# Optimization experiments

Hardware: AMD Instinct MI355X
Metric: run time of the kernel (lower is better)

## Reference

```python
import jax, jax.numpy as jnp
import numpy as np

BS, NS, D, H = 4, 1024, 2048, 16
DH = D // H
SCALE = DH ** -0.5
MASK_BIAS = -1e9


def setup_inputs() -> dict:
    key = jax.random.key(0)
    k1, k2, k3, k4, k5 = jax.random.split(key, 5)
    x = jax.random.normal(k1, (BS, NS, D), dtype=jnp.float32)
    attention_ids = jax.random.randint(k2, (BS, NS), 0, 2, dtype=jnp.int32)
    # torch.nn.Linear weights: [out_features, in_features]
    w_in = jax.random.normal(k3, (3 * D, D), dtype=jnp.float32) * (D ** -0.5)
    w_out = jax.random.normal(k4, (D, D), dtype=jnp.float32) * (D ** -0.5)
    b_out = jax.random.normal(k5, (D,), dtype=jnp.float32) * 0.02
    return {"x": x, "attention_ids": attention_ids, "w_in": w_in,
            "w_out": w_out, "b_out": b_out}


def reference(x, attention_ids, w_in, w_out, b_out):
    bs, ns, _ = x.shape
    qkv = jnp.einsum('bsd,ed->bse', x, w_in)            # [bs, ns, 3*D]
    qkv = qkv.reshape(bs, ns, 3, H, DH).transpose(2, 0, 3, 1, 4)
    q, k, v = qkv[0], qkv[1], qkv[2]                     # [bs, H, ns, DH]
    attn = jnp.einsum('bhqd,bhkd->bhqk', q, k)           # [bs, H, ns, ns]
    # NOTE: mask bias added BEFORE the scale multiply, as in the source.
    bias = (attention_ids.astype(attn.dtype) * MASK_BIAS)[:, None, None, :]
    attn = jax.nn.softmax((attn + bias) * SCALE, axis=-1)
    out = jnp.einsum('bhqk,bhkd->bhqd', attn, v)         # [bs, H, ns, DH]
    out = out.transpose(0, 2, 1, 3).reshape(bs, ns, D)
    return jnp.einsum('bsd,ed->bse', out, w_out) + b_out
```

## Files before the change

### kernel.cpp

```cpp
#include <hip/hip_runtime.h>
#include <hip/hip_bf16.h>
#include <stdint.h>

typedef __bf16 bf16;
typedef __bf16 bf16x8 __attribute__((ext_vector_type(8)));
typedef __bf16 bf16x4 __attribute__((ext_vector_type(4)));
typedef float floatx4 __attribute__((ext_vector_type(4)));

#define NSEQ   1024
#define DM     2048
#define NH     16
#define DHD    128
#define E3     6144
#define SCALE_F 0.08838834764831845f
#define MBIAS_S (-1.0e9f * SCALE_F)
#define NEG_HUGE (-3.0e38f)

static __device__ __forceinline__ floatx4 mfma16(bf16x8 a, bf16x8 b, floatx4 c) {
  return __builtin_amdgcn_mfma_f32_16x16x32_bf16(a, b, c, 0, 0, 0);
}

static __device__ __forceinline__ void load_lds16(const bf16* g, bf16* l) {
  __builtin_amdgcn_global_load_lds(
      (__attribute__((address_space(1))) const void*)g,
      (__attribute__((address_space(3))) void*)l, 16, 0, 0);
}

#define SCHED0 __builtin_amdgcn_sched_barrier(0)

__global__ __launch_bounds__(256) void cast_bf16_kernel(const float* __restrict__ in,
                                                        bf16* __restrict__ out) {
  int i = blockIdx.x * 256 + threadIdx.x;
  float4 v = ((const float4*)in)[i];
  bf16x4 o;
  o[0] = (bf16)v.x; o[1] = (bf16)v.y; o[2] = (bf16)v.z; o[3] = (bf16)v.w;
  ((bf16x4*)out)[i] = o;
}

template <typename OutT>
__global__ __launch_bounds__(512) void gemm256_bt_kernel(
    const bf16* __restrict__ A, const bf16* __restrict__ B,
    OutT* __restrict__ C, const float* __restrict__ bias,
    int N, int K) {
  __shared__ __align__(16) bf16 Al[2][2][256 * 32];
  __shared__ __align__(16) bf16 Bl[2][2][256 * 32];
  const int NT = K >> 6;
  const int ntn = N >> 8;
  const int tm = blockIdx.x / ntn;
  const int tn = blockIdx.x - tm * ntn;
  const int tid = threadIdx.x;
  const int w = tid >> 6, lane = tid & 63;
  const int lq = lane & 15, lg = lane >> 4;
  const int wr = w >> 2, wc = w & 3;
  const int sub = lane >> 2;
  const int cpl = (lane & 3) ^ ((lane >> 3) & 3);
  const int scp8 = (lg ^ ((lq >> 1) & 3)) << 3;

  const bf16* Ag = A + (size_t)(tm * 256) * K;
  const bf16* Bg = B + (size_t)(tn * 256) * K;

  auto STAGE = [&](const bf16* G, bf16* Ldst, int kcol) {
#pragma unroll
    for (int j = 0; j < 2; j++) {
      const int r0 = w * 32 + j * 16;
      load_lds16(G + (size_t)(r0 + sub) * K + kcol + cpl * 8, Ldst + r0 * 32);
    }
  };
  auto RD = [&](const bf16* slot, int rbase) -> bf16x8 {
    return *(const bf16x8*)(slot + (rbase + lq) * 32 + scp8);
  };

  floatx4 acc[8][4] = {};

  STAGE(Ag, Al[0][0], 0);
  STAGE(Bg, Bl[0][0], 0);
  STAGE(Ag, Al[0][1], 32);
  STAGE(Bg, Bl[0][1], 32);
  STAGE(Ag, Al[1][0], 64);
  STAGE(Bg, Bl[1][0], 64);
  asm volatile("s_waitcnt vmcnt(8)" ::: "memory");
  SCHED0;
  __builtin_amdgcn_s_barrier();
  SCHED0;

  int buf = 0;
  for (int kt = 0; kt < NT; ++kt) {
    const int nb = buf ^ 1;
    const int k1 = ((kt + 1 < NT) ? kt + 1 : NT - 1) << 6;
    const int k2 = ((kt + 2 < NT) ? kt + 2 : NT - 1) << 6;
    bf16x8 af[4], bfr[4];

#pragma unroll
    for (int ni = 0; ni < 4; ni++) bfr[ni] = RD(Bl[buf][0], wc * 64 + ni * 16);
#pragma unroll
    for (int mi = 0; mi < 4; mi++) af[mi] = RD(Al[buf][0], wr * 128 + mi * 16);
    STAGE(Ag, Al[nb][1], k1 + 32);
    SCHED0; __builtin_amdgcn_s_barrier();
    asm volatile("s_waitcnt lgkmcnt(0)" ::: "memory"); SCHED0;
    __builtin_amdgcn_s_setprio(1);
#pragma unroll
    for (int mi = 0; mi < 4; mi++)
#pragma unroll
      for (int ni = 0; ni < 4; ni++)
        acc[mi][ni] = mfma16(af[mi], bfr[ni], acc[mi][ni]);
    __builtin_amdgcn_s_setprio(0);
    SCHED0; __builtin_amdgcn_s_barrier(); SCHED0;

#pragma unroll
    for (int mi = 0; mi < 4; mi++)
      af[mi] = RD(Al[buf][0], wr * 128 + (4 + mi) * 16);
    STAGE(Bg, Bl[nb][1], k1 + 32);
    SCHED0; __builtin_amdgcn_s_barrier();
    asm volatile("s_waitcnt lgkmcnt(0)" ::: "memory"); SCHED0;
    __builtin_amdgcn_s_setprio(1);
#pragma unroll
    for (int mi = 0; mi < 4; mi++)
#pragma unroll
      for (int ni = 0; ni < 4; ni++)
        acc[4 + mi][ni] = mfma16(af[mi], bfr[ni], acc[4 + mi][ni]);
    __builtin_amdgcn_s_setprio(0);
    asm volatile("s_waitcnt vmcnt(8)" ::: "memory");
    SCHED0; __builtin_amdgcn_s_barrier(); SCHED0;

#pragma unroll
    for (int ni = 0; ni < 4; ni++) bfr[ni] = RD(Bl[buf][1], wc * 64 + ni * 16);
#pragma unroll
    for (int mi = 0; mi < 4; mi++) af[mi] = RD(Al[buf][1], wr * 128 + mi * 16);
    STAGE(Ag, Al[buf][0], k2);
    SCHED0; __builtin_amdgcn_s_barrier();
    asm volatile("s_waitcnt lgkmcnt(0)" ::: "memory"); SCHED0;
    __builtin_amdgcn_s_setprio(1);
#pragma unroll
    for (int mi = 0; mi < 4; mi++)
#pragma unroll
      for (int ni = 0; ni < 4; ni++)
        acc[mi][ni] = mfma16(af[mi], bfr[ni], acc[mi][ni]);
    __builtin_amdgcn_s_setprio(0);
    SCHED0; __builtin_amdgcn_s_barrier(); SCHED0;

#pragma unroll
    for (int mi = 0; mi < 4; mi++)
      af[mi] = RD(Al[buf][1], wr * 128 + (4 + mi) * 16);
    STAGE(Bg, Bl[buf][0], k2);
    SCHED0; __builtin_amdgcn_s_barrier();
    asm volatile("s_waitcnt lgkmcnt(0)" ::: "memory"); SCHED0;
    __builtin_amdgcn_s_setprio(1);
#pragma unroll
    for (int mi = 0; mi < 4; mi++)
#pragma unroll
      for (int ni = 0; ni < 4; ni++)
        acc[4 + mi][ni] = mfma16(af[mi], bfr[ni], acc[4 + mi][ni]);
    __builtin_amdgcn_s_setprio(0);
    asm volatile("s_waitcnt vmcnt(8)" ::: "memory");
    SCHED0; __builtin_amdgcn_s_barrier(); SCHED0;

    buf = nb;
  }
  asm volatile("s_waitcnt vmcnt(0)" ::: "memory");

#pragma unroll
  for (int ni = 0; ni < 4; ni++) {
    const int col = tn * 256 + wc * 64 + ni * 16 + lq;
    const float bv = bias ? bias[col] : 0.f;
#pragma unroll
    for (int m = 0; m < 8; m++) {
      const size_t rb = (size_t)(tm * 256 + wr * 128 + m * 16 + lg * 4);
#pragma unroll
      for (int r = 0; r < 4; r++)
        C[(rb + r) * N + col] = (OutT)(acc[m][ni][r] + bv);
    }
  }
}

template <typename OutT>
__global__ __launch_bounds__(256) void gemm_bt_kernel(
    const bf16* __restrict__ A, const bf16* __restrict__ B,
    OutT* __restrict__ C, const float* __restrict__ bias,
    int N, int K) {
  __shared__ bf16 As[128 * 32];
  __shared__ bf16 Bs[128 * 32];
  const int ntn = N >> 7;
  const int tm = blockIdx.x / ntn;
  const int tn = blockIdx.x - tm * ntn;
  const int tid = threadIdx.x;
  const int w = tid >> 6;
  const int lane = tid & 63;
  const int lq = lane & 15;
  const int lg = lane >> 4;
  const int wr = w >> 1;
  const int wc = w & 1;

  const bf16* Ag = A + (size_t)(tm * 128) * K;
  const bf16* Bg = B + (size_t)(tn * 128) * K;
  const int c0 = tid, c1 = tid + 256;
  const int r0 = c0 >> 2, o0 = (c0 & 3) * 8;
  const int r1 = c1 >> 2, o1 = (c1 & 3) * 8;
  bf16* lA0 = As + w * 512;
  bf16* lA1 = As + w * 512 + 2048;
  bf16* lB0 = Bs + w * 512;
  bf16* lB1 = Bs + w * 512 + 2048;

  floatx4 acc[4][4] = {};

  for (int k0 = 0; k0 < K; k0 += 32) {
    load_lds16(Ag + (size_t)r0 * K + k0 + o0, lA0);
    load_lds16(Ag + (size_t)r1 * K + k0 + o1, lA1);
    load_lds16(Bg + (size_t)r0 * K + k0 + o0, lB0);
    load_lds16(Bg + (size_t)r1 * K + k0 + o1, lB1);
    __syncthreads();
    bf16x8 af[4], bfr[4];
#pragma unroll
    for (int m = 0; m < 4; m++)
      af[m] = *(const bf16x8*)(As + (wr * 64 + m * 16 + lq) * 32 + lg * 8);
#pragma unroll
    for (int n = 0; n < 4; n++)
      bfr[n] = *(const bf16x8*)(Bs + (wc * 64 + n * 16 + lq) * 32 + lg * 8);
#pragma unroll
    for (int m = 0; m < 4; m++)
#pragma unroll
      for (int n = 0; n < 4; n++)
        acc[m][n] = mfma16(af[m], bfr[n], acc[m][n]);
    __syncthreads();
  }

#pragma unroll
  for (int n = 0; n < 4; n++) {
    const int ccol = tn * 128 + wc * 64 + n * 16 + lq;
    const float bv = bias ? bias[ccol] : 0.f;
#pragma unroll
    for (int m = 0; m < 4; m++) {
      const size_t rbase = (size_t)(tm * 128 + wr * 64 + m * 16 + lg * 4);
#pragma unroll
      for (int r = 0; r < 4; r++)
        C[(rbase + r) * N + ccol] = (OutT)(acc[m][n][r] + bv);
    }
  }
}

__global__ __launch_bounds__(256) void vtrans_kernel(const bf16* __restrict__ qkv,
                                                     bf16* __restrict__ vt) {
  const int bid = blockIdx.x;
  const int sblk = bid & 7;
  const int h = (bid >> 3) & 15;
  const int b = bid >> 7;
  const int t = threadIdx.x;
  const int dhb = (t & 7) | (((t >> 6) & 1) << 3);
  const int sb  = ((t >> 3) & 7) | (((t >> 7) & 1) << 3);
  const int s0 = sblk * 128 + sb * 8;
  const int dh0 = dhb * 8;
  const bf16* src = qkv + (size_t)(b * NSEQ + s0) * E3 + 2 * DM + h * DHD + dh0;
  bf16x8 r[8];
#pragma unroll
  for (int i = 0; i < 8; i++) r[i] = *(const bf16x8*)(src + (size_t)i * E3);
  bf16* dst = vt + ((size_t)(b * NH + h) * DHD + dh0) * NSEQ + s0;
#pragma unroll
  for (int j = 0; j < 8; j++) {
    bf16x8 o;
#pragma unroll
    for (int i = 0; i < 8; i++) o[i] = r[i][j];
    *(bf16x8*)(dst + (size_t)j * NSEQ) = o;
  }
}

__global__ __launch_bounds__(256) void attn_kernel(
    const bf16* __restrict__ qkv, const bf16* __restrict__ vt,
    const int* __restrict__ ids, bf16* __restrict__ ao) {
  __shared__ bf16 Ksh[2][64 * 128];
  __shared__ bf16 Vsh[2][128 * 64];
  __shared__ bf16 plds[4][16][72];
  const int bid = blockIdx.x;
  const int qt = bid & 15;
  const int h = (bid >> 4) & 15;
  const int b = bid >> 8;
  const int tid = threadIdx.x;
  const int w = tid >> 6;
  const int lane = tid & 63;
  const int lq = lane & 15;
  const int lg = lane >> 4;
  const int q0 = qt * 64 + w * 16;
  const int swz = (lq & 7) << 4;

  const int krow0 = w * 16 + (lane >> 4);
  const int kc = lane & 15;
  const int vrow0 = w * 32 + (lane >> 3);
  const int vc = lane & 7;
  const int vr7 = (lane >> 3) & 7;

  const bf16* kg = qkv + DM + h * DHD;
  const bf16* vg = vt + (size_t)(b * NH + h) * DHD * NSEQ;

  auto stage = [&](int buf, int k0) {
#pragma unroll
    for (int i = 0; i < 4; i++) {
      const int kr = krow0 + i * 4;
      load_lds16(kg + (size_t)(b * NSEQ + k0 + kr) * E3 + ((kc ^ (kr & 7)) * 8),
                 &Ksh[buf][(w * 16 + i * 4) * 128]);
    }
#pragma unroll
    for (int i = 0; i < 4; i++) {
      const int vr = vrow0 + i * 8;
      load_lds16(vg + (size_t)vr * NSEQ + k0 + ((vc ^ vr7) * 8),
                 &Vsh[buf][(w * 32 + i * 8) * 64]);
    }
  };

  bf16x8 qf[4];
  const bf16* qb = qkv + (size_t)(b * NSEQ + q0 + lq) * E3 + h * DHD + lg * 8;
#pragma unroll
  for (int kk = 0; kk < 4; kk++) qf[kk] = *(const bf16x8*)(qb + kk * 32);

  floatx4 acc[8] = {};
  float M[4], L[4];
#pragma unroll
  for (int r = 0; r < 4; r++) { M[r] = NEG_HUGE; L[r] = 0.f; }

  bf16 (*pw)[72] = plds[w];
  const int* idb = ids + b * NSEQ;

  stage(0, 0);
  __syncthreads();
  int cur = 0;

  for (int t = 0; t < 16; t++) {
    const int k0 = t * 64;
    if (t < 15) stage(cur ^ 1, k0 + 64);

    const bf16* Kc = Ksh[cur];
    floatx4 s[4] = {};
#pragma unroll
    for (int n = 0; n < 4; n++) {
      const int krow = n * 16 + lq;
#pragma unroll
      for (int kk = 0; kk < 4; kk++) {
        bf16x8 kf = *(const bf16x8*)(Kc + krow * 128 +
                                     (((kk * 64 + lg * 16) ^ swz) >> 1));
        s[n] = mfma16(qf[kk], kf, s[n]);
      }
    }
    float sa[4][4], pm[4];
#pragma unroll
    for (int r = 0; r < 4; r++) pm[r] = NEG_HUGE;
#pragma unroll
    for (int n = 0; n < 4; n++) {
      const float bv = idb[k0 + n * 16 + lq] ? MBIAS_S : 0.f;
#pragma unroll
      for (int r = 0; r < 4; r++) {
        sa[n][r] = s[n][r] * SCALE_F + bv;
        pm[r] = fmaxf(pm[r], sa[n][r]);
      }
    }
#pragma unroll
    for (int m = 1; m <= 8; m <<= 1)
#pragma unroll
      for (int r = 0; r < 4; r++) pm[r] = fmaxf(pm[r], __shfl_xor(pm[r], m, 64));
    float corr[4];
#pragma unroll
    for (int r = 0; r < 4; r++) {
      const float mn = fmaxf(M[r], pm[r]);
      corr[r] = __expf(M[r] - mn);
      M[r] = mn;
    }
    float rs[4] = {0.f, 0.f, 0.f, 0.f};
#pragma unroll
    for (int n = 0; n < 4; n++)
#pragma unroll
      for (int r = 0; r < 4; r++) {
        const float p = __expf(sa[n][r] - M[r]);
        sa[n][r] = p;
        rs[r] += p;
      }
#pragma unroll
    for (int m = 1; m <= 8; m <<= 1)
#pragma unroll
      for (int r = 0; r < 4; r++) rs[r] += __shfl_xor(rs[r], m, 64);
#pragma unroll
    for (int r = 0; r < 4; r++) L[r] = L[r] * corr[r] + rs[r];
#pragma unroll
    for (int n8 = 0; n8 < 8; n8++)
#pragma unroll
      for (int r = 0; r < 4; r++) acc[n8][r] *= corr[r];
#pragma unroll
    for (int n = 0; n < 4; n++)
#pragma unroll
      for (int r = 0; r < 4; r++) pw[lg * 4 + r][n * 16 + lq] = (bf16)sa[n][r];
    bf16x8 pf0 = *(const bf16x8*)(&pw[lq][lg * 8]);
    bf16x8 pf1 = *(const bf16x8*)(&pw[lq][32 + lg * 8]);
    const bf16* Vc = Vsh[cur];
#pragma unroll
    for (int n8 = 0; n8 < 8; n8++) {
      const int vrow = n8 * 16 + lq;
      bf16x8 v0 = *(const bf16x8*)(Vc + vrow * 64 + (((lg * 16) ^ swz) >> 1));
      bf16x8 v1 = *(const bf16x8*)(Vc + vrow * 64 + (((64 + lg * 16) ^ swz) >> 1));
      acc[n8] = mfma16(pf0, v0, acc[n8]);
      acc[n8] = mfma16(pf1, v1, acc[n8]);
    }
    __syncthreads();
    cur ^= 1;
  }

  float inv[4];
#pragma unroll
  for (int r = 0; r < 4; r++) inv[r] = 1.f / L[r];
  bf16* aob = ao + (size_t)(b * NSEQ + q0 + lg * 4) * DM + h * DHD + lq;
#pragma unroll
  for (int n8 = 0; n8 < 8; n8++)
#pragma unroll
    for (int r = 0; r < 4; r++)
      aob[(size_t)r * DM + n8 * 16] = (bf16)(acc[n8][r] * inv[r]);
}

extern "C" void kernel_launch(void* const* d_in, const int* in_sizes, int n_in,
                              void* d_out, int out_size, void* d_ws, size_t ws_size,
                              hipStream_t stream) {
  const float* x     = (const float*)d_in[0];
  const int*   ids   = (const int*)d_in[1];
  const float* w_in  = (const float*)d_in[2];
  const float* w_out = (const float*)d_in[3];
  const float* b_out = (const float*)d_in[4];
  float* out = (float*)d_out;

  bf16* ws  = (bf16*)d_ws;
  bf16* xb  = ws;
  bf16* wib = xb  + (size_t)4096 * 2048;
  bf16* wob = wib + (size_t)6144 * 2048;
  bf16* qkv = wob + (size_t)2048 * 2048;
  bf16* vtb = qkv + (size_t)4096 * 6144;
  bf16* aob = vtb + (size_t)4 * 16 * 128 * 1024;

  cast_bf16_kernel<<<8192, 256, 0, stream>>>(x, xb);
  cast_bf16_kernel<<<12288, 256, 0, stream>>>(w_in, wib);
  cast_bf16_kernel<<<4096, 256, 0, stream>>>(w_out, wob);
  gemm256_bt_kernel<bf16><<<16 * 24, 512, 0, stream>>>(xb, wib, qkv, nullptr, 6144, 2048);
  vtrans_kernel<<<512, 256, 0, stream>>>(qkv, vtb);
  attn_kernel<<<1024, 256, 0, stream>>>(qkv, vtb, ids, aob);
  gemm_bt_kernel<float><<<32 * 16, 256, 0, stream>>>(aob, wob, out, b_out, 2048, 2048);
}
```

Baseline: 325.9 us.

## Merge cast kernels, restructure GEMM k-loop phases, defer softmax rescaling

```diff
diff --git a/kernel.cpp b/kernel.cpp
--- a/kernel.cpp
+++ b/kernel.cpp
@@ -15,6 +15,7 @@
 #define SCALE_F 0.08838834764831845f
 #define MBIAS_S (-1.0e9f * SCALE_F)
 #define NEG_HUGE (-3.0e38f)
+#define DEFER_THR 8.0f
 
 static __device__ __forceinline__ floatx4 mfma16(bf16x8 a, bf16x8 b, floatx4 c) {
   return __builtin_amdgcn_mfma_f32_16x16x32_bf16(a, b, c, 0, 0, 0);
@@ -28,13 +29,22 @@
 
 #define SCHED0 __builtin_amdgcn_sched_barrier(0)
 
-__global__ __launch_bounds__(256) void cast_bf16_kernel(const float* __restrict__ in,
-                                                        bf16* __restrict__ out) {
-  int i = blockIdx.x * 256 + threadIdx.x;
-  float4 v = ((const float4*)in)[i];
+__global__ __launch_bounds__(256) void cast3_kernel(
+    const float* __restrict__ x, const float* __restrict__ wi,
+    const float* __restrict__ wo, bf16* __restrict__ xb,
+    bf16* __restrict__ wib, bf16* __restrict__ wob) {
+  const int blk = blockIdx.x;
+  const float* src;
+  bf16* dst;
+  int base;
+  if (blk < 8192)       { src = x;  dst = xb;  base = blk; }
+  else if (blk < 20480) { src = wi; dst = wib; base = blk - 8192; }
+  else                  { src = wo; dst = wob; base = blk - 20480; }
+  const int i = base * 256 + threadIdx.x;
+  float4 v = ((const float4*)src)[i];
   bf16x4 o;
   o[0] = (bf16)v.x; o[1] = (bf16)v.y; o[2] = (bf16)v.z; o[3] = (bf16)v.w;
-  ((bf16x4*)out)[i] = o;
+  ((bf16x4*)dst)[i] = o;
 }
 
 template <typename OutT>
@@ -88,68 +98,42 @@
     const int nb = buf ^ 1;
     const int k1 = ((kt + 1 < NT) ? kt + 1 : NT - 1) << 6;
     const int k2 = ((kt + 2 < NT) ? kt + 2 : NT - 1) << 6;
-    bf16x8 af[4], bfr[4];
+    bf16x8 af[8], bfr[4];
 
 #pragma unroll
     for (int ni = 0; ni < 4; ni++) bfr[ni] = RD(Bl[buf][0], wc * 64 + ni * 16);
 #pragma unroll
-    for (int mi = 0; mi < 4; mi++) af[mi] = RD(Al[buf][0], wr * 128 + mi * 16);
+    for (int mi = 0; mi < 8; mi++) af[mi] = RD(Al[buf][0], wr * 128 + mi * 16);
     STAGE(Ag, Al[nb][1], k1 + 32);
+    STAGE(Bg, Bl[nb][1], k1 + 32);
+    asm volatile("s_waitcnt lgkmcnt(8)" ::: "memory");
     SCHED0; __builtin_amdgcn_s_barrier();
     asm volatile("s_waitcnt lgkmcnt(0)" ::: "memory"); SCHED0;
     __builtin_amdgcn_s_setprio(1);
 #pragma unroll
-    for (int mi = 0; mi < 4; mi++)
+    for (int mi = 0; mi < 8; mi++)
 #pragma unroll
       for (int ni = 0; ni < 4; ni++)
         acc[mi][ni] = mfma16(af[mi], bfr[ni], acc[mi][ni]);
     __builtin_amdgcn_s_setprio(0);
+    asm volatile("s_waitcnt vmcnt(8)" ::: "memory");
     SCHED0; __builtin_amdgcn_s_barrier(); SCHED0;
 
 #pragma unroll
-    for (int mi = 0; mi < 4; mi++)
-      af[mi] = RD(Al[buf][0], wr * 128 + (4 + mi) * 16);
-    STAGE(Bg, Bl[nb][1], k1 + 32);
+    for (int ni = 0; ni < 4; ni++) bfr[ni] = RD(Bl[buf][1], wc * 64 + ni * 16);
+#pragma unroll
+    for (int mi = 0; mi < 8; mi++) af[mi] = RD(Al[buf][1], wr * 128 + mi * 16);
+    STAGE(Ag, Al[buf][0], k2);
+    STAGE(Bg, Bl[buf][0], k2);
+    asm volatile("s_waitcnt lgkmcnt(8)" ::: "memory");
     SCHED0; __builtin_amdgcn_s_barrier();
     asm volatile("s_waitcnt lgkmcnt(0)" ::: "memory"); SCHED0;
     __builtin_amdgcn_s_setprio(1);
 #pragma unroll
-    for (int mi = 0; mi < 4; mi++)
-#pragma unroll
-      for (int ni = 0; ni < 4; ni++)
-        acc[4 + mi][ni] = mfma16(af[mi], bfr[ni], acc[4 + mi][ni]);
-    __builtin_amdgcn_s_setprio(0);
-    asm volatile("s_waitcnt vmcnt(8)" ::: "memory");
-    SCHED0; __builtin_amdgcn_s_barrier(); SCHED0;
-
-#pragma unroll
-    for (int ni = 0; ni < 4; ni++) bfr[ni] = RD(Bl[buf][1], wc * 64 + ni * 16);
-#pragma unroll
-    for (int mi = 0; mi < 4; mi++) af[mi] = RD(Al[buf][1], wr * 128 + mi * 16);
-    STAGE(Ag, Al[buf][0], k2);
-    SCHED0; __builtin_amdgcn_s_barrier();
-    asm volatile("s_waitcnt lgkmcnt(0)" ::: "memory"); SCHED0;
-    __builtin_amdgcn_s_setprio(1);
-#pragma unroll
-    for (int mi = 0; mi < 4; mi++)
+    for (int mi = 0; mi < 8; mi++)
 #pragma unroll
       for (int ni = 0; ni < 4; ni++)
         acc[mi][ni] = mfma16(af[mi], bfr[ni], acc[mi][ni]);
-    __builtin_amdgcn_s_setprio(0);
-    SCHED0; __builtin_amdgcn_s_barrier(); SCHED0;
-
-#pragma unroll
-    for (int mi = 0; mi < 4; mi++)
-      af[mi] = RD(Al[buf][1], wr * 128 + (4 + mi) * 16);
-    STAGE(Bg, Bl[buf][0], k2);
-    SCHED0; __builtin_amdgcn_s_barrier();
-    asm volatile("s_waitcnt lgkmcnt(0)" ::: "memory"); SCHED0;
-    __builtin_amdgcn_s_setprio(1);
-#pragma unroll
-    for (int mi = 0; mi < 4; mi++)
-#pragma unroll
-      for (int ni = 0; ni < 4; ni++)
-        acc[4 + mi][ni] = mfma16(af[mi], bfr[ni], acc[4 + mi][ni]);
     __builtin_amdgcn_s_setprio(0);
     asm volatile("s_waitcnt vmcnt(8)" ::: "memory");
     SCHED0; __builtin_amdgcn_s_barrier(); SCHED0;
@@ -327,6 +311,7 @@
 
     const bf16* Kc = Ksh[cur];
     floatx4 s[4] = {};
+    __builtin_amdgcn_s_setprio(1);
 #pragma unroll
     for (int n = 0; n < 4; n++) {
       const int krow = n * 16 + lq;
@@ -337,6 +322,7 @@
         s[n] = mfma16(qf[kk], kf, s[n]);
       }
     }
+    __builtin_amdgcn_s_setprio(0);
     float sa[4][4], pm[4];
 #pragma unroll
     for (int r = 0; r < 4; r++) pm[r] = NEG_HUGE;
@@ -353,12 +339,19 @@
     for (int m = 1; m <= 8; m <<= 1)
 #pragma unroll
       for (int r = 0; r < 4; r++) pm[r] = fmaxf(pm[r], __shfl_xor(pm[r], m, 64));
+
+    int grew = 0;
+#pragma unroll
+    for (int r = 0; r < 4; r++) grew |= (pm[r] > M[r] + DEFER_THR) ? 1 : 0;
+    const bool full = __any(grew);
     float corr[4];
-#pragma unroll
-    for (int r = 0; r < 4; r++) {
-      const float mn = fmaxf(M[r], pm[r]);
-      corr[r] = __expf(M[r] - mn);
-      M[r] = mn;
+    if (full) {
+#pragma unroll
+      for (int r = 0; r < 4; r++) {
+        const float mn = fmaxf(M[r], pm[r]);
+        corr[r] = __expf(M[r] - mn);
+        M[r] = mn;
+      }
     }
     float rs[4] = {0.f, 0.f, 0.f, 0.f};
 #pragma unroll
@@ -373,12 +366,17 @@
     for (int m = 1; m <= 8; m <<= 1)
 #pragma unroll
       for (int r = 0; r < 4; r++) rs[r] += __shfl_xor(rs[r], m, 64);
-#pragma unroll
-    for (int r = 0; r < 4; r++) L[r] = L[r] * corr[r] + rs[r];
-#pragma unroll
-    for (int n8 = 0; n8 < 8; n8++)
-#pragma unroll
-      for (int r = 0; r < 4; r++) acc[n8][r] *= corr[r];
+    if (full) {
+#pragma unroll
+      for (int r = 0; r < 4; r++) L[r] = L[r] * corr[r] + rs[r];
+#pragma unroll
+      for (int n8 = 0; n8 < 8; n8++)
+#pragma unroll
+        for (int r = 0; r < 4; r++) acc[n8][r] *= corr[r];
+    } else {
+#pragma unroll
+      for (int r = 0; r < 4; r++) L[r] += rs[r];
+    }
 #pragma unroll
     for (int n = 0; n < 4; n++)
 #pragma unroll
@@ -386,6 +384,7 @@
     bf16x8 pf0 = *(const bf16x8*)(&pw[lq][lg * 8]);
     bf16x8 pf1 = *(const bf16x8*)(&pw[lq][32 + lg * 8]);
     const bf16* Vc = Vsh[cur];
+    __builtin_amdgcn_s_setprio(1);
 #pragma unroll
     for (int n8 = 0; n8 < 8; n8++) {
       const int vrow = n8 * 16 + lq;
@@ -394,6 +393,7 @@
       acc[n8] = mfma16(pf0, v0, acc[n8]);
       acc[n8] = mfma16(pf1, v1, acc[n8]);
     }
+    __builtin_amdgcn_s_setprio(0);
     __syncthreads();
     cur ^= 1;
   }
@@ -427,9 +427,7 @@
   bf16* vtb = qkv + (size_t)4096 * 6144;
   bf16* aob = vtb + (size_t)4 * 16 * 128 * 1024;
 
-  cast_bf16_kernel<<<8192, 256, 0, stream>>>(x, xb);
-  cast_bf16_kernel<<<12288, 256, 0, stream>>>(w_in, wib);
-  cast_bf16_kernel<<<4096, 256, 0, stream>>>(w_out, wob);
+  cast3_kernel<<<24576, 256, 0, stream>>>(x, w_in, w_out, xb, wib, wob);
   gemm256_bt_kernel<bf16><<<16 * 24, 512, 0, stream>>>(xb, wib, qkv, nullptr, 6144, 2048);
   vtrans_kernel<<<512, 256, 0, stream>>>(qkv, vtb);
   attn_kernel<<<1024, 256, 0, stream>>>(qkv, vtb, ids, aob);
```

Result: faster. 304.4 us (-6.6%).
